# Performance work log

Measured on AMD Instinct MI355X. Metric: run time of the kernel, lower is better.

## Reference

```python
import jax, jax.numpy as jnp
import numpy as np

B, S, E, H = 4, 2048, 1024, 16
D = E // H  # head_dim = 64

def setup_inputs() -> dict:
    key = jax.random.key(0)
    k1, k2, k3 = jax.random.split(key, 3)
    x = jax.random.normal(k1, (B, S, E), dtype=jnp.float32)
    # Linear weights stored as [in, out] so y = x @ W (torch Linear uses W^T; same math).
    w_att = jax.random.normal(k2, (E, 3 * E), dtype=jnp.float32) * (1.0 / np.sqrt(E))
    w_proj = jax.random.normal(k3, (E, E), dtype=jnp.float32) * (1.0 / np.sqrt(E))
    return {"x": x, "w_att": w_att, "w_proj": w_proj}

def reference(x, w_att, w_proj):
    b, s, e = x.shape
    qkv = x @ w_att                      # [b, s, 3e]
    q, k, v = jnp.split(qkv, 3, axis=-1)
    # [b, h, s, d]
    q = q.reshape(b, s, H, D).transpose(0, 2, 1, 3)
    k = k.reshape(b, s, H, D).transpose(0, 2, 1, 3)
    v = v.reshape(b, s, H, D).transpose(0, 2, 1, 3)
    scale = 1.0 / np.sqrt(D)
    att = jnp.einsum('bhqd,bhkd->bhqk', q, k) * scale  # [b, h, s, s]
    causal = jnp.tril(jnp.ones((s, s), dtype=bool))
    att = jnp.where(causal[None, None], att, jnp.finfo(att.dtype).min)
    att = jax.nn.softmax(att, axis=-1)
    y = jnp.einsum('bhqk,bhkd->bhqd', att, v)          # [b, h, s, d]
    y = y.transpose(0, 2, 1, 3).reshape(b, s, e)
    return y @ w_proj
```

## Files before the change

kernel.cpp:

```cpp
#include <hip/hip_runtime.h>
#include <hip/hip_bf16.h>

typedef __bf16 b16v8 __attribute__((ext_vector_type(8)));
typedef __bf16 b16v4 __attribute__((ext_vector_type(4)));
typedef float  f32x4 __attribute__((ext_vector_type(4)));

#define BB 4
#define SS 2048
#define EE 1024
#define HH 16
#define DD 64

#define QSCALE 0.18033688011112042f
#define CMAX 20.0f

__device__ __forceinline__ void async16(const __bf16* g, __bf16* l) {
  typedef __attribute__((address_space(1))) const unsigned int gu32;
  typedef __attribute__((address_space(3))) unsigned int lu32;
  __builtin_amdgcn_global_load_lds((gu32*)g, (lu32*)l, 16, 0, 0);
}

__device__ __forceinline__ f32x4 mfma16x16x16_bf16(b16v4 a, b16v4 b, f32x4 c) {
#if __has_builtin(__builtin_amdgcn_mfma_f32_16x16x16_bf16)
  return __builtin_amdgcn_mfma_f32_16x16x16_bf16(a, b, c, 0, 0, 0);
#else
  typedef short s16v4 __attribute__((ext_vector_type(4)));
  union U { b16v4 h; s16v4 s; };
  U ua, ub; ua.h = a; ub.h = b;
  return __builtin_amdgcn_mfma_f32_16x16x16bf16_1k(ua.s, ub.s, c, 0, 0, 0);
#endif
}

__global__ __launch_bounds__(256) void prep_kernel(const float* __restrict__ x,
                                                   __bf16* __restrict__ xb,
                                                   const float* __restrict__ w_att,
                                                   __bf16* __restrict__ watt,
                                                   const float* __restrict__ w_proj,
                                                   __bf16* __restrict__ wproj) {
  __shared__ float t[32][33];
  const int bid = blockIdx.x;
  if (bid < 8192) {
    int i = bid * 256 + threadIdx.x;
    float4 f = ((const float4*)x)[i];
    b16v4 o = {(__bf16)f.x, (__bf16)f.y, (__bf16)f.z, (__bf16)f.w};
    ((b16v4*)xb)[i] = o;
    return;
  }
  const float* w;
  __bf16* wt;
  int N, local;
  if (bid < 11264) { w = w_att; wt = watt; N = 3072; local = bid - 8192; }
  else             { w = w_proj; wt = wproj; N = 1024; local = bid - 11264; }
  const int K = 1024;
  int n0 = (local % (N >> 5)) * 32, k0 = (local / (N >> 5)) * 32;
  int tx = threadIdx.x & 31, ty = threadIdx.x >> 5;
#pragma unroll
  for (int j = 0; j < 32; j += 8)
    t[ty + j][tx] = w[(size_t)(k0 + ty + j) * N + n0 + tx];
  __syncthreads();
#pragma unroll
  for (int j = 0; j < 32; j += 8)
    wt[(size_t)(n0 + ty + j) * K + k0 + tx] = (__bf16)t[tx][ty + j];
}

__global__ __launch_bounds__(256) void gemm_qkv(const __bf16* __restrict__ A,
                                                const __bf16* __restrict__ Bt,
                                                __bf16* __restrict__ qb,
                                                __bf16* __restrict__ kb,
                                                __bf16* __restrict__ vtb,
                                                int K) {
  __shared__ __bf16 a_lds[2][256 * 32];
  __shared__ __bf16 b_lds[2][128 * 32];
  const int tid = threadIdx.x;
  const int lane = tid & 63;
  const int w = tid >> 6;
  const int wm = (w >> 1) * 128, wn = (w & 1) * 64;
  const int l16 = lane & 15, quad = lane >> 4;

  const int gx = gridDim.x;
  const int nwg = gx * gridDim.y;
  const int bid0 = blockIdx.y * gx + blockIdx.x;
  const int qq = nwg >> 3;
  const int xcd = bid0 & 7, idx = bid0 >> 3;
  const int wgid = xcd * qq + idx;
  const int bxx = wgid % gx, byy = wgid / gx;

  const __bf16* Ab = A + (size_t)byy * 256 * K;
  const __bf16* Bb = Bt + (size_t)bxx * 128 * K;

  auto stage = [&](int k0, int bufi) {
#pragma unroll
    for (int i = 0; i < 4; ++i) {
      int c = tid + i * 256;
      int row = c >> 2, ch = c & 3;
      async16(Ab + (size_t)row * K + k0 + ((ch ^ (row & 3)) * 8), a_lds[bufi] + c * 8);
    }
#pragma unroll
    for (int i = 0; i < 2; ++i) {
      int c = tid + i * 256;
      int row = c >> 2, ch = c & 3;
      async16(Bb + (size_t)row * K + k0 + ((ch ^ (row & 3)) * 8), b_lds[bufi] + c * 8);
    }
  };

  f32x4 acc[8][4];
#pragma unroll
  for (int i = 0; i < 8; ++i)
#pragma unroll
    for (int j = 0; j < 4; ++j) acc[i][j] = f32x4{0.f, 0.f, 0.f, 0.f};

  stage(0, 0);
  const int KT = K >> 5;
  const int sw = (quad ^ (l16 & 3)) * 8;
  for (int kt = 0; kt < KT; ++kt) {
    __syncthreads();
    if (kt + 1 < KT) stage((kt + 1) << 5, (kt + 1) & 1);
    const __bf16* ab = a_lds[kt & 1];
    const __bf16* bb = b_lds[kt & 1];
    b16v8 af[8], bf4[4];
#pragma unroll
    for (int t = 0; t < 8; ++t)
      af[t] = *(const b16v8*)(ab + (wm + t * 16 + l16) * 32 + sw);
#pragma unroll
    for (int t = 0; t < 4; ++t)
      bf4[t] = *(const b16v8*)(bb + (wn + t * 16 + l16) * 32 + sw);
#pragma unroll
    for (int mt = 0; mt < 8; ++mt)
#pragma unroll
      for (int nt = 0; nt < 4; ++nt)
        acc[mt][nt] = __builtin_amdgcn_mfma_f32_16x16x32_bf16(af[mt], bf4[nt], acc[mt][nt], 0, 0, 0);
  }

#pragma unroll
  for (int mt = 0; mt < 8; ++mt)
#pragma unroll
    for (int nt = 0; nt < 4; ++nt) {
      int row = byy * 256 + wm + mt * 16 + quad * 4;
      int col = bxx * 128 + wn + nt * 16 + l16;
      int b = row >> 11, s = row & 2047;
      int sec = col >> 10, cc = col & 1023;
      int h = cc >> 6, d = cc & 63;
      if (sec == 2) {
        b16v4 vv = {(__bf16)acc[mt][nt][0], (__bf16)acc[mt][nt][1],
                    (__bf16)acc[mt][nt][2], (__bf16)acc[mt][nt][3]};
        *(b16v4*)(vtb + ((size_t)(b * HH + h) * DD + d) * SS + s) = vv;
      } else {
        __bf16* dst = (sec == 0) ? qb : kb;
        float sc = (sec == 0) ? QSCALE : 1.0f;
#pragma unroll
        for (int r = 0; r < 4; ++r)
          dst[(((size_t)(b * HH + h) * SS + s + r) << 6) + d] = (__bf16)(acc[mt][nt][r] * sc);
      }
    }
}

__global__ __launch_bounds__(256) void gemm_proj(const __bf16* __restrict__ A,
                                                 const __bf16* __restrict__ Bt,
                                                 float* __restrict__ out,
                                                 int N, int K) {
  __shared__ __bf16 a_lds[2][128 * 32];
  __shared__ __bf16 b_lds[2][64 * 32];
  const int tid = threadIdx.x;
  const int lane = tid & 63;
  const int w = tid >> 6;
  const int wm = (w >> 1) * 64, wn = (w & 1) * 32;
  const int l16 = lane & 15, quad = lane >> 4;

  const int gx = gridDim.x;
  const int nwg = gx * gridDim.y;
  const int bid0 = blockIdx.y * gx + blockIdx.x;
  const int qq = nwg >> 3;
  const int xcd = bid0 & 7, idx = bid0 >> 3;
  const int wgid = xcd * qq + idx;
  const int bxx = wgid % gx, byy = wgid / gx;

  const __bf16* Ab = A + (size_t)byy * 128 * K;
  const __bf16* Bb = Bt + (size_t)bxx * 64 * K;

  auto stage = [&](int k0, int bufi) {
#pragma unroll
    for (int i = 0; i < 2; ++i) {
      int c = tid + i * 256;
      int row = c >> 2, ch = c & 3;
      async16(Ab + (size_t)row * K + k0 + ((ch ^ (row & 3)) * 8), a_lds[bufi] + c * 8);
    }
    {
      int c = tid;
      int row = c >> 2, ch = c & 3;
      async16(Bb + (size_t)row * K + k0 + ((ch ^ (row & 3)) * 8), b_lds[bufi] + c * 8);
    }
  };

  f32x4 acc[4][2];
#pragma unroll
  for (int i = 0; i < 4; ++i)
#pragma unroll
    for (int j = 0; j < 2; ++j) acc[i][j] = f32x4{0.f, 0.f, 0.f, 0.f};

  stage(0, 0);
  const int KT = K >> 5;
  const int sw = (quad ^ (l16 & 3)) * 8;
  for (int kt = 0; kt < KT; ++kt) {
    __syncthreads();
    if (kt + 1 < KT) stage((kt + 1) << 5, (kt + 1) & 1);
    const __bf16* ab = a_lds[kt & 1];
    const __bf16* bb = b_lds[kt & 1];
    b16v8 af[4], bf4[2];
#pragma unroll
    for (int t = 0; t < 4; ++t)
      af[t] = *(const b16v8*)(ab + (wm + t * 16 + l16) * 32 + sw);
#pragma unroll
    for (int t = 0; t < 2; ++t)
      bf4[t] = *(const b16v8*)(bb + (wn + t * 16 + l16) * 32 + sw);
#pragma unroll
    for (int mt = 0; mt < 4; ++mt)
#pragma unroll
      for (int nt = 0; nt < 2; ++nt)
        acc[mt][nt] = __builtin_amdgcn_mfma_f32_16x16x32_bf16(af[mt], bf4[nt], acc[mt][nt], 0, 0, 0);
  }

#pragma unroll
  for (int mt = 0; mt < 4; ++mt)
#pragma unroll
    for (int nt = 0; nt < 2; ++nt)
#pragma unroll
      for (int r = 0; r < 4; ++r) {
        int row = byy * 128 + wm + mt * 16 + quad * 4 + r;
        int col = bxx * 64 + wn + nt * 16 + l16;
        out[(size_t)row * N + col] = acc[mt][nt][r];
      }
}

__global__ __launch_bounds__(256, 4) void attn_kernel(const __bf16* __restrict__ qb,
                                                      const __bf16* __restrict__ kb,
                                                      const __bf16* __restrict__ vtb,
                                                      __bf16* __restrict__ y) {
  __shared__ __bf16 kv_lds[2][8192];
  const int tid = threadIdx.x;
  const int lane = tid & 63;
  const int w = tid >> 6;
  const int l16 = lane & 15, quad = lane >> 4;
  const int bh = blockIdx.x, p = blockIdx.y;
  const int b = bh >> 4, h = bh & 15;
  const __bf16* kbase = kb + (size_t)bh * SS * DD;
  const __bf16* vtbase = vtb + (size_t)bh * DD * SS;

  const int e = l16 & 7;
  const int koff0 = l16 * 64 + ((quad ^ e) * 8);
  const int koff1 = l16 * 64 + (((quad + 4) ^ e) * 8);
  int voff[4];
#pragma unroll
  for (int kf = 0; kf < 4; ++kf)
    voff[kf] = 4096 + l16 * 64 + (((kf * 2 + (quad >> 1)) ^ e) * 8) + ((quad & 1) * 4);

  int gK[2], gV[2], lK[2], lV[2];
#pragma unroll
  for (int i = 0; i < 2; ++i) {
    int L = tid + i * 256;
    int row = L >> 3, c = L & 7;
    gK[i] = row * DD + ((c ^ (row & 7)) * 8);
    lK[i] = L * 8;
    gV[i] = row * SS + ((c ^ (row & 7)) * 8);
    lV[i] = 4096 + L * 8;
  }
  auto stage = [&](int j, __bf16* buf) {
    const __bf16* kj = kbase + j * (64 * DD);
    const __bf16* vj = vtbase + j * 64;
#pragma unroll
    for (int i = 0; i < 2; ++i) async16(kj + gK[i], buf + lK[i]);
#pragma unroll
    for (int i = 0; i < 2; ++i) async16(vj + gV[i], buf + lV[i]);
  };

#pragma unroll
  for (int t = 0; t < 2; ++t) {
    const int qt = (t == 0) ? (31 - p) : p;

    b16v8 qf[2];
#pragma unroll
    for (int ks = 0; ks < 2; ++ks)
      qf[ks] = *(const b16v8*)(qb + ((size_t)bh * SS + qt * 64 + w * 16 + l16) * DD + ks * 32 + quad * 8);

    f32x4 o[4];
#pragma unroll
    for (int dt = 0; dt < 4; ++dt) o[dt] = f32x4{0.f, 0.f, 0.f, 0.f};
    f32x4 lv = {0.f, 0.f, 0.f, 0.f};

    __syncthreads();
    stage(0, kv_lds[0]);

    for (int j = 0; j <= qt; ++j) {
      __syncthreads();
      if (j < qt) stage(j + 1, kv_lds[(j + 1) & 1]);
      const __bf16* buf = kv_lds[0] + ((j & 1) << 13);

      f32x4 s[4];
#pragma unroll
      for (int kf = 0; kf < 4; ++kf) s[kf] = f32x4{-CMAX, -CMAX, -CMAX, -CMAX};
      __builtin_amdgcn_s_setprio(1);
#pragma unroll
      for (int kf = 0; kf < 4; ++kf) {
        b16v8 k0 = *(const b16v8*)(buf + koff0 + kf * 1024);
        b16v8 k1 = *(const b16v8*)(buf + koff1 + kf * 1024);
        s[kf] = __builtin_amdgcn_mfma_f32_16x16x32_bf16(k0, qf[0], s[kf], 0, 0, 0);
        s[kf] = __builtin_amdgcn_mfma_f32_16x16x32_bf16(k1, qf[1], s[kf], 0, 0, 0);
      }
      __builtin_amdgcn_s_setprio(0);
      if (j == qt) {
        int ql = w * 16 + l16;
#pragma unroll
        for (int kf = 0; kf < 4; ++kf)
#pragma unroll
          for (int r = 0; r < 4; ++r)
            if (kf * 16 + quad * 4 + r > ql) s[kf][r] = -1e30f;
      }
#pragma unroll
      for (int kf = 0; kf < 4; ++kf)
#pragma unroll
        for (int r = 0; r < 4; ++r) s[kf][r] = __builtin_amdgcn_exp2f(s[kf][r]);
      lv += (s[0] + s[1]) + (s[2] + s[3]);
      __builtin_amdgcn_s_setprio(1);
#pragma unroll
      for (int kf = 0; kf < 4; ++kf) {
        b16v4 pf = {(__bf16)s[kf][0], (__bf16)s[kf][1], (__bf16)s[kf][2], (__bf16)s[kf][3]};
#pragma unroll
        for (int dt = 0; dt < 4; ++dt) {
          b16v4 vf = *(const b16v4*)(buf + voff[kf] + dt * 1024);
          o[dt] = mfma16x16x16_bf16(vf, pf, o[dt]);
        }
      }
      __builtin_amdgcn_s_setprio(0);
    }

    float lr = (lv[0] + lv[1]) + (lv[2] + lv[3]);
    lr += __shfl_xor(lr, 16);
    lr += __shfl_xor(lr, 32);
    float inv = 1.0f / lr;
    int q = qt * 64 + w * 16 + l16;
#pragma unroll
    for (int dt = 0; dt < 4; ++dt) {
      b16v4 ov = {(__bf16)(o[dt][0] * inv), (__bf16)(o[dt][1] * inv),
                  (__bf16)(o[dt][2] * inv), (__bf16)(o[dt][3] * inv)};
      *(b16v4*)(y + ((size_t)b * SS + q) * EE + h * 64 + dt * 16 + quad * 4) = ov;
    }
  }
}

extern "C" void kernel_launch(void* const* d_in, const int* in_sizes, int n_in,
                              void* d_out, int out_size, void* d_ws, size_t ws_size,
                              hipStream_t stream) {
  (void)in_sizes; (void)n_in; (void)out_size; (void)ws_size;
  const float* x = (const float*)d_in[0];
  const float* w_att = (const float*)d_in[1];
  const float* w_proj = (const float*)d_in[2];
  float* out = (float*)d_out;

  char* ws = (char*)d_ws;
  size_t off = 0;
  auto alloc = [&](size_t elems) { __bf16* p = (__bf16*)(ws + off); off += elems * 2; return p; };
  __bf16* xb = alloc(8388608);
  __bf16* qb = alloc(8388608);
  __bf16* kb = alloc(8388608);
  __bf16* vtb = alloc(8388608);
  __bf16* watt = alloc(3145728);
  __bf16* wproj = alloc(1048576);

  prep_kernel<<<12288, 256, 0, stream>>>(x, xb, w_att, watt, w_proj, wproj);
  gemm_qkv<<<dim3(24, 32), 256, 0, stream>>>(xb, watt, qb, kb, vtb, 1024);
  attn_kernel<<<dim3(64, 16), 256, 0, stream>>>(qb, kb, vtb, xb);
  gemm_proj<<<dim3(16, 64), 256, 0, stream>>>(xb, wproj, out, 1024, 1024);
}
```

Measured before the change: 274.4 us.

## Retile QKV GEMM, deepen proj K-step, use 128-row query tiles in attention

The QKV GEMM M-tile is halved to 128 rows, which doubles the grid and halves accumulator registers. The projection GEMM now stages 64-wide K slices with an 8-way XOR swizzle, halving the number of barrier iterations. The attention kernel drops the paired causal-balanced tiles of 64 queries and instead gives each 512-thread block one 128-query tile, with 8 waves sharing every K/V stage and per-wave causal masking on the last two KV tiles. This trades the old load balancing across causal tiles for more reuse of each K/V load, but now processes tiles from longest to shortest, so blocks finish unevenly.

```diff
diff --git a/kernel.cpp b/kernel.cpp
--- a/kernel.cpp
+++ b/kernel.cpp
@@ -69,12 +69,12 @@
                                                 __bf16* __restrict__ kb,
                                                 __bf16* __restrict__ vtb,
                                                 int K) {
-  __shared__ __bf16 a_lds[2][256 * 32];
+  __shared__ __bf16 a_lds[2][128 * 32];
   __shared__ __bf16 b_lds[2][128 * 32];
   const int tid = threadIdx.x;
   const int lane = tid & 63;
   const int w = tid >> 6;
-  const int wm = (w >> 1) * 128, wn = (w & 1) * 64;
+  const int wm = (w >> 1) * 64, wn = (w & 1) * 64;
   const int l16 = lane & 15, quad = lane >> 4;
 
   const int gx = gridDim.x;
@@ -85,12 +85,12 @@
   const int wgid = xcd * qq + idx;
   const int bxx = wgid % gx, byy = wgid / gx;
 
-  const __bf16* Ab = A + (size_t)byy * 256 * K;
+  const __bf16* Ab = A + (size_t)byy * 128 * K;
   const __bf16* Bb = Bt + (size_t)bxx * 128 * K;
 
   auto stage = [&](int k0, int bufi) {
 #pragma unroll
-    for (int i = 0; i < 4; ++i) {
+    for (int i = 0; i < 2; ++i) {
       int c = tid + i * 256;
       int row = c >> 2, ch = c & 3;
       async16(Ab + (size_t)row * K + k0 + ((ch ^ (row & 3)) * 8), a_lds[bufi] + c * 8);
@@ -103,9 +103,9 @@
     }
   };
 
-  f32x4 acc[8][4];
-#pragma unroll
-  for (int i = 0; i < 8; ++i)
+  f32x4 acc[4][4];
+#pragma unroll
+  for (int i = 0; i < 4; ++i)
 #pragma unroll
     for (int j = 0; j < 4; ++j) acc[i][j] = f32x4{0.f, 0.f, 0.f, 0.f};
 
@@ -117,25 +117,24 @@
     if (kt + 1 < KT) stage((kt + 1) << 5, (kt + 1) & 1);
     const __bf16* ab = a_lds[kt & 1];
     const __bf16* bb = b_lds[kt & 1];
-    b16v8 af[8], bf4[4];
-#pragma unroll
-    for (int t = 0; t < 8; ++t)
+    b16v8 af[4], bf4[4];
+#pragma unroll
+    for (int t = 0; t < 4; ++t) {
       af[t] = *(const b16v8*)(ab + (wm + t * 16 + l16) * 32 + sw);
-#pragma unroll
-    for (int t = 0; t < 4; ++t)
       bf4[t] = *(const b16v8*)(bb + (wn + t * 16 + l16) * 32 + sw);
-#pragma unroll
-    for (int mt = 0; mt < 8; ++mt)
+    }
+#pragma unroll
+    for (int mt = 0; mt < 4; ++mt)
 #pragma unroll
       for (int nt = 0; nt < 4; ++nt)
         acc[mt][nt] = __builtin_amdgcn_mfma_f32_16x16x32_bf16(af[mt], bf4[nt], acc[mt][nt], 0, 0, 0);
   }
 
 #pragma unroll
-  for (int mt = 0; mt < 8; ++mt)
+  for (int mt = 0; mt < 4; ++mt)
 #pragma unroll
     for (int nt = 0; nt < 4; ++nt) {
-      int row = byy * 256 + wm + mt * 16 + quad * 4;
+      int row = byy * 128 + wm + mt * 16 + quad * 4;
       int col = bxx * 128 + wn + nt * 16 + l16;
       int b = row >> 11, s = row & 2047;
       int sec = col >> 10, cc = col & 1023;
@@ -158,8 +157,8 @@
                                                  const __bf16* __restrict__ Bt,
                                                  float* __restrict__ out,
                                                  int N, int K) {
-  __shared__ __bf16 a_lds[2][128 * 32];
-  __shared__ __bf16 b_lds[2][64 * 32];
+  __shared__ __bf16 a_lds[2][128 * 64];
+  __shared__ __bf16 b_lds[2][64 * 64];
   const int tid = threadIdx.x;
   const int lane = tid & 63;
   const int w = tid >> 6;
@@ -179,15 +178,16 @@
 
   auto stage = [&](int k0, int bufi) {
 #pragma unroll
+    for (int i = 0; i < 4; ++i) {
+      int c = tid + i * 256;
+      int row = c >> 3, ch = c & 7;
+      async16(Ab + (size_t)row * K + k0 + ((ch ^ (row & 7)) * 8), a_lds[bufi] + c * 8);
+    }
+#pragma unroll
     for (int i = 0; i < 2; ++i) {
       int c = tid + i * 256;
-      int row = c >> 2, ch = c & 3;
-      async16(Ab + (size_t)row * K + k0 + ((ch ^ (row & 3)) * 8), a_lds[bufi] + c * 8);
-    }
-    {
-      int c = tid;
-      int row = c >> 2, ch = c & 3;
-      async16(Bb + (size_t)row * K + k0 + ((ch ^ (row & 3)) * 8), b_lds[bufi] + c * 8);
+      int row = c >> 3, ch = c & 7;
+      async16(Bb + (size_t)row * K + k0 + ((ch ^ (row & 7)) * 8), b_lds[bufi] + c * 8);
     }
   };
 
@@ -198,25 +198,33 @@
     for (int j = 0; j < 2; ++j) acc[i][j] = f32x4{0.f, 0.f, 0.f, 0.f};
 
   stage(0, 0);
-  const int KT = K >> 5;
-  const int sw = (quad ^ (l16 & 3)) * 8;
+  const int KT = K >> 6;
+  const int e7 = l16 & 7;
+  const int swz0 = (quad ^ e7) * 8;
+  const int swz1 = ((4 + quad) ^ e7) * 8;
   for (int kt = 0; kt < KT; ++kt) {
     __syncthreads();
-    if (kt + 1 < KT) stage((kt + 1) << 5, (kt + 1) & 1);
+    if (kt + 1 < KT) stage((kt + 1) << 6, (kt + 1) & 1);
     const __bf16* ab = a_lds[kt & 1];
     const __bf16* bb = b_lds[kt & 1];
-    b16v8 af[4], bf4[2];
-#pragma unroll
-    for (int t = 0; t < 4; ++t)
-      af[t] = *(const b16v8*)(ab + (wm + t * 16 + l16) * 32 + sw);
-#pragma unroll
-    for (int t = 0; t < 2; ++t)
-      bf4[t] = *(const b16v8*)(bb + (wn + t * 16 + l16) * 32 + sw);
+    b16v8 af[4][2], bf[2][2];
+#pragma unroll
+    for (int t = 0; t < 4; ++t) {
+      af[t][0] = *(const b16v8*)(ab + (wm + t * 16 + l16) * 64 + swz0);
+      af[t][1] = *(const b16v8*)(ab + (wm + t * 16 + l16) * 64 + swz1);
+    }
+#pragma unroll
+    for (int t = 0; t < 2; ++t) {
+      bf[t][0] = *(const b16v8*)(bb + (wn + t * 16 + l16) * 64 + swz0);
+      bf[t][1] = *(const b16v8*)(bb + (wn + t * 16 + l16) * 64 + swz1);
+    }
 #pragma unroll
     for (int mt = 0; mt < 4; ++mt)
 #pragma unroll
       for (int nt = 0; nt < 2; ++nt)
-        acc[mt][nt] = __builtin_amdgcn_mfma_f32_16x16x32_bf16(af[mt], bf4[nt], acc[mt][nt], 0, 0, 0);
+#pragma unroll
+        for (int ks = 0; ks < 2; ++ks)
+          acc[mt][nt] = __builtin_amdgcn_mfma_f32_16x16x32_bf16(af[mt][ks], bf[nt][ks], acc[mt][nt], 0, 0, 0);
   }
 
 #pragma unroll
@@ -231,7 +239,7 @@
       }
 }
 
-__global__ __launch_bounds__(256, 4) void attn_kernel(const __bf16* __restrict__ qb,
+__global__ __launch_bounds__(512, 4) void attn_kernel(const __bf16* __restrict__ qb,
                                                       const __bf16* __restrict__ kb,
                                                       const __bf16* __restrict__ vtb,
                                                       __bf16* __restrict__ y) {
@@ -240,7 +248,8 @@
   const int lane = tid & 63;
   const int w = tid >> 6;
   const int l16 = lane & 15, quad = lane >> 4;
-  const int bh = blockIdx.x, p = blockIdx.y;
+  const int bh = blockIdx.x;
+  const int qt = 15 - blockIdx.y;
   const int b = bh >> 4, h = bh & 15;
   const __bf16* kbase = kb + (size_t)bh * SS * DD;
   const __bf16* vtbase = vtb + (size_t)bh * DD * SS;
@@ -253,96 +262,90 @@
   for (int kf = 0; kf < 4; ++kf)
     voff[kf] = 4096 + l16 * 64 + (((kf * 2 + (quad >> 1)) ^ e) * 8) + ((quad & 1) * 4);
 
-  int gK[2], gV[2], lK[2], lV[2];
-#pragma unroll
-  for (int i = 0; i < 2; ++i) {
-    int L = tid + i * 256;
-    int row = L >> 3, c = L & 7;
-    gK[i] = row * DD + ((c ^ (row & 7)) * 8);
-    lK[i] = L * 8;
-    gV[i] = row * SS + ((c ^ (row & 7)) * 8);
-    lV[i] = 4096 + L * 8;
-  }
+  const int srow = tid >> 3, sc = tid & 7;
+  const int gK = srow * DD + ((sc ^ (srow & 7)) * 8);
+  const int gV = srow * SS + ((sc ^ (srow & 7)) * 8);
+  const int lL = tid * 8;
   auto stage = [&](int j, __bf16* buf) {
-    const __bf16* kj = kbase + j * (64 * DD);
-    const __bf16* vj = vtbase + j * 64;
-#pragma unroll
-    for (int i = 0; i < 2; ++i) async16(kj + gK[i], buf + lK[i]);
-#pragma unroll
-    for (int i = 0; i < 2; ++i) async16(vj + gV[i], buf + lV[i]);
+    async16(kbase + j * (64 * DD) + gK, buf + lL);
+    async16(vtbase + j * 64 + gV, buf + 4096 + lL);
   };
 
-#pragma unroll
-  for (int t = 0; t < 2; ++t) {
-    const int qt = (t == 0) ? (31 - p) : p;
-
-    b16v8 qf[2];
-#pragma unroll
-    for (int ks = 0; ks < 2; ++ks)
-      qf[ks] = *(const b16v8*)(qb + ((size_t)bh * SS + qt * 64 + w * 16 + l16) * DD + ks * 32 + quad * 8);
-
-    f32x4 o[4];
-#pragma unroll
-    for (int dt = 0; dt < 4; ++dt) o[dt] = f32x4{0.f, 0.f, 0.f, 0.f};
-    f32x4 lv = {0.f, 0.f, 0.f, 0.f};
-
+  b16v8 qf[2];
+#pragma unroll
+  for (int ks = 0; ks < 2; ++ks)
+    qf[ks] = *(const b16v8*)(qb + ((size_t)bh * SS + qt * 128 + w * 16 + l16) * DD + ks * 32 + quad * 8);
+
+  f32x4 o[4];
+#pragma unroll
+  for (int dt = 0; dt < 4; ++dt) o[dt] = f32x4{0.f, 0.f, 0.f, 0.f};
+  f32x4 lv = {0.f, 0.f, 0.f, 0.f};
+
+  stage(0, kv_lds[0]);
+  const int jmax = 2 * qt + 1;
+  for (int j = 0; j <= jmax; ++j) {
     __syncthreads();
-    stage(0, kv_lds[0]);
-
-    for (int j = 0; j <= qt; ++j) {
-      __syncthreads();
-      if (j < qt) stage(j + 1, kv_lds[(j + 1) & 1]);
-      const __bf16* buf = kv_lds[0] + ((j & 1) << 13);
-
-      f32x4 s[4];
-#pragma unroll
-      for (int kf = 0; kf < 4; ++kf) s[kf] = f32x4{-CMAX, -CMAX, -CMAX, -CMAX};
-      __builtin_amdgcn_s_setprio(1);
-#pragma unroll
-      for (int kf = 0; kf < 4; ++kf) {
-        b16v8 k0 = *(const b16v8*)(buf + koff0 + kf * 1024);
-        b16v8 k1 = *(const b16v8*)(buf + koff1 + kf * 1024);
-        s[kf] = __builtin_amdgcn_mfma_f32_16x16x32_bf16(k0, qf[0], s[kf], 0, 0, 0);
-        s[kf] = __builtin_amdgcn_mfma_f32_16x16x32_bf16(k1, qf[1], s[kf], 0, 0, 0);
+    if (j < jmax) stage(j + 1, kv_lds[(j + 1) & 1]);
+    const __bf16* buf = kv_lds[0] + ((j & 1) << 13);
+
+    if (j == jmax && w < 4) continue;
+
+    f32x4 s[4];
+#pragma unroll
+    for (int kf = 0; kf < 4; ++kf) s[kf] = f32x4{-CMAX, -CMAX, -CMAX, -CMAX};
+    __builtin_amdgcn_s_setprio(1);
+#pragma unroll
+    for (int kf = 0; kf < 4; ++kf) {
+      b16v8 k0 = *(const b16v8*)(buf + koff0 + kf * 1024);
+      b16v8 k1 = *(const b16v8*)(buf + koff1 + kf * 1024);
+      s[kf] = __builtin_amdgcn_mfma_f32_16x16x32_bf16(k0, qf[0], s[kf], 0, 0, 0);
+      s[kf] = __builtin_amdgcn_mfma_f32_16x16x32_bf16(k1, qf[1], s[kf], 0, 0, 0);
+    }
+    __builtin_amdgcn_s_setprio(0);
+    if (j == 2 * qt && w < 4) {
+      int ql = w * 16 + l16;
+#pragma unroll
+      for (int kf = 0; kf < 4; ++kf)
+#pragma unroll
+        for (int r = 0; r < 4; ++r)
+          if (kf * 16 + quad * 4 + r > ql) s[kf][r] = -1e30f;
+    }
+    if (j == jmax && w >= 4) {
+      int ql = (w - 4) * 16 + l16;
+#pragma unroll
+      for (int kf = 0; kf < 4; ++kf)
+#pragma unroll
+        for (int r = 0; r < 4; ++r)
+          if (kf * 16 + quad * 4 + r > ql) s[kf][r] = -1e30f;
+    }
+#pragma unroll
+    for (int kf = 0; kf < 4; ++kf)
+#pragma unroll
+      for (int r = 0; r < 4; ++r) s[kf][r] = __builtin_amdgcn_exp2f(s[kf][r]);
+    lv += (s[0] + s[1]) + (s[2] + s[3]);
+    __builtin_amdgcn_s_setprio(1);
+#pragma unroll
+    for (int kf = 0; kf < 4; ++kf) {
+      b16v4 pf = {(__bf16)s[kf][0], (__bf16)s[kf][1], (__bf16)s[kf][2], (__bf16)s[kf][3]};
+#pragma unroll
+      for (int dt = 0; dt < 4; ++dt) {
+        b16v4 vf = *(const b16v4*)(buf + voff[kf] + dt * 1024);
+        o[dt] = mfma16x16x16_bf16(vf, pf, o[dt]);
       }
-      __builtin_amdgcn_s_setprio(0);
-      if (j == qt) {
-        int ql = w * 16 + l16;
-#pragma unroll
-        for (int kf = 0; kf < 4; ++kf)
-#pragma unroll
-          for (int r = 0; r < 4; ++r)
-            if (kf * 16 + quad * 4 + r > ql) s[kf][r] = -1e30f;
-      }
-#pragma unroll
-      for (int kf = 0; kf < 4; ++kf)
-#pragma unroll
-        for (int r = 0; r < 4; ++r) s[kf][r] = __builtin_amdgcn_exp2f(s[kf][r]);
-      lv += (s[0] + s[1]) + (s[2] + s[3]);
-      __builtin_amdgcn_s_setprio(1);
-#pragma unroll
-      for (int kf = 0; kf < 4; ++kf) {
-        b16v4 pf = {(__bf16)s[kf][0], (__bf16)s[kf][1], (__bf16)s[kf][2], (__bf16)s[kf][3]};
-#pragma unroll
-        for (int dt = 0; dt < 4; ++dt) {
-          b16v4 vf = *(const b16v4*)(buf + voff[kf] + dt * 1024);
-          o[dt] = mfma16x16x16_bf16(vf, pf, o[dt]);
-        }
-      }
-      __builtin_amdgcn_s_setprio(0);
-    }
-
-    float lr = (lv[0] + lv[1]) + (lv[2] + lv[3]);
-    lr += __shfl_xor(lr, 16);
-    lr += __shfl_xor(lr, 32);
-    float inv = 1.0f / lr;
-    int q = qt * 64 + w * 16 + l16;
-#pragma unroll
-    for (int dt = 0; dt < 4; ++dt) {
-      b16v4 ov = {(__bf16)(o[dt][0] * inv), (__bf16)(o[dt][1] * inv),
-                  (__bf16)(o[dt][2] * inv), (__bf16)(o[dt][3] * inv)};
-      *(b16v4*)(y + ((size_t)b * SS + q) * EE + h * 64 + dt * 16 + quad * 4) = ov;
-    }
+    }
+    __builtin_amdgcn_s_setprio(0);
+  }
+
+  float lr = (lv[0] + lv[1]) + (lv[2] + lv[3]);
+  lr += __shfl_xor(lr, 16);
+  lr += __shfl_xor(lr, 32);
+  float inv = 1.0f / lr;
+  int q = qt * 128 + w * 16 + l16;
+#pragma unroll
+  for (int dt = 0; dt < 4; ++dt) {
+    b16v4 ov = {(__bf16)(o[dt][0] * inv), (__bf16)(o[dt][1] * inv),
+                (__bf16)(o[dt][2] * inv), (__bf16)(o[dt][3] * inv)};
+    *(b16v4*)(y + ((size_t)b * SS + q) * EE + h * 64 + dt * 16 + quad * 4) = ov;
   }
 }
 
@@ -366,7 +369,7 @@
   __bf16* wproj = alloc(1048576);
 
   prep_kernel<<<12288, 256, 0, stream>>>(x, xb, w_att, watt, w_proj, wproj);
-  gemm_qkv<<<dim3(24, 32), 256, 0, stream>>>(xb, watt, qb, kb, vtb, 1024);
-  attn_kernel<<<dim3(64, 16), 256, 0, stream>>>(qb, kb, vtb, xb);
+  gemm_qkv<<<dim3(24, 64), 256, 0, stream>>>(xb, watt, qb, kb, vtb, 1024);
+  attn_kernel<<<dim3(64, 16), 512, 0, stream>>>(qb, kb, vtb, xb);
   gemm_proj<<<dim3(16, 64), 256, 0, stream>>>(xb, wproj, out, 1024, 1024);
 }
```

Result: faster. 240.8 us (-12.2%).
